# Optimization experiments

Hardware: AMD Instinct MI355X
Metric: run time of the kernel (lower is better)

## Reference

```python
import jax, jax.numpy as jnp
import numpy as np

EPS = 1e-5  # torch nn.LayerNorm default


def layer_norm(x, g, b):
    mu = jnp.mean(x, axis=-1, keepdims=True)
    var = jnp.mean(jnp.square(x - mu), axis=-1, keepdims=True)
    return (x - mu) * jax.lax.rsqrt(var + EPS) * g + b


def run_dir(g_ih_seq, w_hh, g_hh, b_hh, g_ho, b_ho, reverse):
    """Run one LayerNormLSTMCell direction over precomputed LN(x @ W_ih^T).
    g_ih_seq: [S, B, 4H]. Returns final hidden [B, H]."""
    S, B, G = g_ih_seq.shape
    H = G // 4

    def step(carry, gih_t):
        h, c = carry
        gates = gih_t + layer_norm(h @ w_hh.T, g_hh, b_hh)  # [B, 4H]
        i, f, o = jnp.split(jax.nn.sigmoid(gates[:, : 3 * H]), 3, axis=1)
        g = jnp.tanh(gates[:, 3 * H :])
        c = f * c + i * g
        h = o * jnp.tanh(layer_norm(c, g_ho, b_ho))
        return (h, c), None

    z = jnp.zeros((B, H), g_ih_seq.dtype)
    (hT, _), _ = jax.lax.scan(step, (z, z), g_ih_seq, reverse=reverse)
    return hT


def lnlstm(x, w_ih0, w_hh0, ln_ih0_g, ln_ih0_b, ln_hh0_g, ln_hh0_b, ln_ho0_g,
           ln_ho0_b, w_ih1, w_hh1, ln_ih1_g, ln_ih1_b, ln_hh1_g, ln_hh1_b,
           ln_ho1_g, ln_ho1_b):
    # x: [B, S, E] -> permute(1,0,2)
    x_seq = jnp.transpose(x, (1, 0, 2))  # [S, B, E]
    S, B, _ = x_seq.shape

    # ---- layer 0 (time-varying input) ----
    g0f = layer_norm(jnp.einsum('sbe,ge->sbg', x_seq, w_ih0[0]), ln_ih0_g[0], ln_ih0_b[0])
    hf = run_dir(g0f, w_hh0[0], ln_hh0_g[0], ln_hh0_b[0], ln_ho0_g[0], ln_ho0_b[0], False)
    g0b = layer_norm(jnp.einsum('sbe,ge->sbg', x_seq, w_ih0[1]), ln_ih0_g[1], ln_ih0_b[1])
    hb = run_dir(g0b, w_hh0[1], ln_hh0_g[1], ln_hh0_b[1], ln_ho0_g[1], ln_ho0_b[1], True)

    # Due to the `[[None]*N]*seq_len` aliasing bug in the original torch code,
    # the next layer's input is the SAME vector at every timestep:
    xc = jnp.concatenate([hf, hb], axis=1)  # [B, 2H]

    # ---- layer 1 (constant input; LN(x@W_ih^T) computed once, broadcast over time) ----
    g1f = layer_norm(xc @ w_ih1[0].T, ln_ih1_g[0], ln_ih1_b[0])
    hf1 = run_dir(jnp.broadcast_to(g1f, (S,) + g1f.shape), w_hh1[0],
                  ln_hh1_g[0], ln_hh1_b[0], ln_ho1_g[0], ln_ho1_b[0], False)
    g1b = layer_norm(xc @ w_ih1[1].T, ln_ih1_g[1], ln_ih1_b[1])
    hb1 = run_dir(jnp.broadcast_to(g1b, (S,) + g1b.shape), w_hh1[1],
                  ln_hh1_g[1], ln_hh1_b[1], ln_ho1_g[1], ln_ho1_b[1], True)

    # y = max over time of identical vectors == the vector itself
    return jnp.concatenate([hf1, hb1], axis=1)  # [B, 2H]


def setup_inputs() -> dict:
    key = jax.random.key(0)
    ks = jax.random.split(key, 20)
    B, S, E, H = 64, 48, 512, 512
    f = jnp.float32
    n = jax.random.normal
    u = jax.random.uniform
    return {
        'x': n(ks[0], (B, S, E), f),
        'text_length': jax.random.randint(ks[1], (B,), 1, S),
        'w_ih0': n(ks[2], (2, 4 * H, E), f) * 0.05,
        'w_hh0': n(ks[3], (2, 4 * H, H), f) * 0.05,
        'ln_ih0_g': u(ks[4], (2, 4 * H), f, 0.5, 1.5),
        'ln_ih0_b': n(ks[5], (2, 4 * H), f) * 0.02,
        'ln_hh0_g': u(ks[6], (2, 4 * H), f, 0.5, 1.5),
        'ln_hh0_b': n(ks[7], (2, 4 * H), f) * 0.02,
        'ln_ho0_g': u(ks[8], (2, H), f, 0.5, 1.5),
        'ln_ho0_b': n(ks[9], (2, H), f) * 0.02,
        'w_ih1': n(ks[10], (2, 4 * H, 2 * H), f) * 0.05,
        'w_hh1': n(ks[11], (2, 4 * H, H), f) * 0.05,
        'ln_ih1_g': u(ks[12], (2, 4 * H), f, 0.5, 1.5),
        'ln_ih1_b': n(ks[13], (2, 4 * H), f) * 0.02,
        'ln_hh1_g': u(ks[14], (2, 4 * H), f, 0.5, 1.5),
        'ln_hh1_b': n(ks[15], (2, 4 * H), f) * 0.02,
        'ln_ho1_g': u(ks[16], (2, H), f, 0.5, 1.5),
        'ln_ho1_b': n(ks[17], (2, H), f) * 0.02,
    }


def reference(x, text_length, w_ih0, w_hh0, ln_ih0_g, ln_ih0_b, ln_hh0_g,
              ln_hh0_b, ln_ho0_g, ln_ho0_b, w_ih1, w_hh1, ln_ih1_g, ln_ih1_b,
              ln_hh1_g, ln_hh1_b, ln_ho1_g, ln_ho1_b):
    # text_length is accepted but unused by the original forward
    return lnlstm(x, w_ih0, w_hh0, ln_ih0_g, ln_ih0_b, ln_hh0_g, ln_hh0_b,
                  ln_ho0_g, ln_ho0_b, w_ih1, w_hh1, ln_ih1_g, ln_ih1_b,
                  ln_hh1_g, ln_hh1_b, ln_ho1_g, ln_ho1_b)
```

## Files before the change

### kernel.cpp

```cpp
#include <hip/hip_runtime.h>
#include <math.h>

#define HH 512
#define BB 64
#define SS 48
#define EE 512
#define G4 2048
#define EPSF 1e-5f
#define AGENT __HIP_MEMORY_SCOPE_AGENT

__device__ __forceinline__ float aload(const float* p) {
  return __hip_atomic_load(p, __ATOMIC_RELAXED, AGENT);
}
__device__ __forceinline__ void astore(float* p, float v) {
  __hip_atomic_store(p, v, __ATOMIC_RELAXED, AGENT);
}

__device__ __forceinline__ float fsigmoid(float x) {
  float t = __builtin_amdgcn_exp2f(x * -1.44269504088896f);
  return __builtin_amdgcn_rcpf(1.f + t);
}
__device__ __forceinline__ float ftanh(float x) {
  x = fminf(fmaxf(x, -10.f), 10.f);
  float t = __builtin_amdgcn_exp2f(x * 2.88539008177793f);
  return (t - 1.f) * __builtin_amdgcn_rcpf(t + 1.f);
}

__device__ __forceinline__ void gsync(int* c, int target) {
  __builtin_amdgcn_s_waitcnt(0);
  __syncthreads();
  if (threadIdx.x == 0) {
    __hip_atomic_fetch_add(c, 1, __ATOMIC_RELEASE, AGENT);
    int spins = 0;
    while (__hip_atomic_load(c, __ATOMIC_RELAXED, AGENT) < target) {
      __builtin_amdgcn_s_sleep(2);
      if (++spins > (1 << 21)) break;
    }
    (void)__hip_atomic_load(c, __ATOMIC_ACQUIRE, AGENT);
  }
  __syncthreads();
}

__global__ __launch_bounds__(256)
void gemm_ih0(const float* __restrict__ x, const float* __restrict__ w_ih0,
              float* __restrict__ G0) {
  __shared__ float As[16][65];
  __shared__ float Bs[16][65];
  const int m0 = blockIdx.y * 64;
  const int d  = m0 / (BB * SS);
  const float* Wm = w_ih0 + (size_t)d * G4 * EE;
  const int bn = blockIdx.x * 64;
  const int tid = threadIdx.x;
  const int lrow = tid >> 2;
  const int lkk  = (tid & 3) << 2;
  const int tx = tid & 15;
  const int ty = tid >> 4;
  int m  = m0 + lrow;
  int r  = m - d * (BB * SS);
  int b  = r / SS;
  int tl = r - b * SS;
  int s  = d ? (SS - 1 - tl) : tl;
  const float* arow = x + ((size_t)b * SS + s) * EE;

  float acc[4][4] = {};
  for (int k0 = 0; k0 < EE; k0 += 16) {
    float4 av = *(const float4*)(arow + k0 + lkk);
    float4 bv = *(const float4*)(Wm + (size_t)(bn + lrow) * EE + k0 + lkk);
    As[lkk+0][lrow] = av.x; As[lkk+1][lrow] = av.y; As[lkk+2][lrow] = av.z; As[lkk+3][lrow] = av.w;
    Bs[lkk+0][lrow] = bv.x; Bs[lkk+1][lrow] = bv.y; Bs[lkk+2][lrow] = bv.z; Bs[lkk+3][lrow] = bv.w;
    __syncthreads();
    #pragma unroll
    for (int k = 0; k < 16; ++k) {
      float a[4], bbv[4];
      #pragma unroll
      for (int i = 0; i < 4; ++i) a[i] = As[k][ty*4+i];
      #pragma unroll
      for (int j = 0; j < 4; ++j) bbv[j] = Bs[k][tx*4+j];
      #pragma unroll
      for (int i = 0; i < 4; ++i)
        #pragma unroll
        for (int j = 0; j < 4; ++j) acc[i][j] += a[i]*bbv[j];
    }
    __syncthreads();
  }
  for (int i = 0; i < 4; ++i)
    for (int j = 0; j < 4; ++j)
      G0[(size_t)(m0 + ty*4 + i) * G4 + bn + tx*4 + j] = acc[i][j];
}

__global__ __launch_bounds__(256)
void ln_rows(float* __restrict__ X, const float* __restrict__ gamma,
             const float* __restrict__ beta, int rows_per_d) {
  __shared__ float red[8];
  const int row = blockIdx.x;
  const int d = row / rows_per_d;
  float* xr = X + (size_t)row * G4;
  const float* gg = gamma + (size_t)d * G4;
  const float* bb = beta  + (size_t)d * G4;
  float s = 0.f, q = 0.f;
  float v[8];
  #pragma unroll
  for (int it = 0; it < 8; ++it) {
    float xv = xr[threadIdx.x + it*256];
    v[it] = xv; s += xv; q += xv*xv;
  }
  #pragma unroll
  for (int off = 32; off > 0; off >>= 1) { s += __shfl_down(s, off); q += __shfl_down(q, off); }
  int lane = threadIdx.x & 63, wid = threadIdx.x >> 6;
  if (lane == 0) { red[wid] = s; red[4+wid] = q; }
  __syncthreads();
  float ts = red[0]+red[1]+red[2]+red[3];
  float tq = red[4]+red[5]+red[6]+red[7];
  float mu = ts * (1.f/G4);
  float rstd = rsqrtf(tq*(1.f/G4) - mu*mu + EPSF);
  #pragma unroll
  for (int it = 0; it < 8; ++it) {
    int jc = threadIdx.x + it*256;
    xr[jc] = (v[it]-mu)*rstd*gg[jc] + bb[jc];
  }
}

__global__ __launch_bounds__(1024, 4)
void persist7(const float* __restrict__ whh, const float* __restrict__ Gbuf,
              long g_row_stride, long g_t_stride,
              const float* __restrict__ lnhg, const float* __restrict__ lnhb,
              const float* __restrict__ lnog, const float* __restrict__ lnob,
              float* cbuf, float* obuf, float* Rpart, float* Cpart,
              int* flagsA, int* flagsB,
              float* fout, int nsteps,
              int mode1, const float* __restrict__ w_ih1,
              const float* __restrict__ xcb, float* g1pre,
              const float* __restrict__ ln_g1, const float* __restrict__ ln_b1,
              int* cnt_pre) {
  __shared__ float hlds[16][1024];
  __shared__ float part[16][8][64];
  __shared__ float redR[16][64];
  __shared__ float bcR[16][2];
  __shared__ float bcC[16][2];
  __shared__ float sred[32];

  const int bb = blockIdx.x;
  const int tid = threadIdx.x;

  if (mode1) {
    const int dp = bb & 1, nbp = bb >> 1;
    const int pb = tid >> 4, ns = tid & 15;
    const int col = nbp*16 + ns;
    const float* xrow = xcb + (size_t)pb * 1024;
    const float* wv_ = w_ih1 + ((size_t)dp*G4 + col) * 1024;
    float a = 0.f;
    for (int k = 0; k < 1024; k += 4) {
      float4 xv = *(const float4*)(xrow + k);
      float4 wv4 = *(const float4*)(wv_ + k);
      a += xv.x*wv4.x + xv.y*wv4.y + xv.z*wv4.z + xv.w*wv4.w;
    }
    astore(g1pre + ((size_t)dp*BB + pb) * G4 + col, a);
    gsync(cnt_pre + 0, 256);
    if (bb < 128) {
      const int ld = bb >> 6;
      float* xr = g1pre + (size_t)bb * G4;
      const float* gg = ln_g1 + (size_t)ld * G4;
      const float* be = ln_b1 + (size_t)ld * G4;
      float v0 = aload(xr + tid), v1 = aload(xr + tid + 1024);
      float s = v0 + v1, q = v0*v0 + v1*v1;
      #pragma unroll
      for (int off = 32; off > 0; off >>= 1) { s += __shfl_down(s, off); q += __shfl_down(q, off); }
      const int wv2 = tid >> 6;
      if ((tid & 63) == 0) { sred[wv2] = s; sred[16+wv2] = q; }
      __syncthreads();
      float ts = 0.f, tq = 0.f;
      #pragma unroll
      for (int i = 0; i < 16; ++i) { ts += sred[i]; tq += sred[16+i]; }
      float mu = ts * (1.f/G4);
      float rstd = rsqrtf(tq*(1.f/G4) - mu*mu + EPSF);
      astore(xr + tid,        (v0-mu)*rstd*gg[tid]      + be[tid]);
      astore(xr + tid + 1024, (v1-mu)*rstd*gg[tid+1024] + be[tid+1024]);
    }
    gsync(cnt_pre + 16, 256);
  }

  const int g  = bb & 7;
  const int d  = g >> 2;
  const int bq = g & 3;
  const int jb = bb >> 3;
  const int rowbase = d*BB + bq*16;
  const int ke = tid >> 6, nl = tid & 63;
  const int ncol = jb*16 + ((nl>>4) << 9) + (nl & 15);
  int* fA = flagsA + g*1024;
  int* fB = flagsB + g*1024;

  float wreg[32];
  {
    const float* wp = whh + ((size_t)d*G4 + ncol)*HH + (size_t)ke*32;
    #pragma unroll
    for (int i = 0; i < 32; ++i) wreg[i] = wp[i];
  }

  const int bl = tid >> 4, jl = tid & 15;
  const int rowc = rowbase + bl;
  const int jc = jb*16 + jl;
  const int scol = tid & 511, srh = tid >> 9;
  const float ogv = lnog[(size_t)d*HH + scol];
  const float obv = lnob[(size_t)d*HH + scol];
  const int row16 = tid >> 5, j32 = tid & 31;
  const int inv_g = (g_t_stride == 0);

  float hg0=0,hg1=0,hg2=0,hg3=0, hb0=0,hb1=0,hb2=0,hb3=0;
  float cg0=0,cg1=0,cg2=0,cg3=0;
  if (tid < 256) {
    const float* lnhg_d = lnhg + (size_t)d*G4;
    const float* lnhb_d = lnhb + (size_t)d*G4;
    hg0 = lnhg_d[jc];        hb0 = lnhb_d[jc];
    hg1 = lnhg_d[HH+jc];     hb1 = lnhb_d[HH+jc];
    hg2 = lnhg_d[2*HH+jc];   hb2 = lnhb_d[2*HH+jc];
    hg3 = lnhg_d[3*HH+jc];   hb3 = lnhb_d[3*HH+jc];
    if (inv_g) {
      const float* gr = Gbuf + (size_t)rowc * g_row_stride;
      cg0 = gr[jc]; cg1 = gr[HH+jc]; cg2 = gr[2*HH+jc]; cg3 = gr[3*HH+jc];
    }
  }
  float creg = 0.f;

  for (int t = 0; t < nsteps; ++t) {
    float cv[8], ovv[8];
    #pragma unroll
    for (int i = 0; i < 8; ++i) {
      int row = i*2 + srh;
      cv[i]  = aload(cbuf + (size_t)(rowbase + row)*512 + scol);
      ovv[i] = aload(obuf + (size_t)(rowbase + row)*512 + scol);
    }
    if (tid < 512) {
      float s = aload(Cpart + ((size_t)(rowbase+row16)*32 + j32)*2 + 0);
      float q = aload(Cpart + ((size_t)(rowbase+row16)*32 + j32)*2 + 1);
      #pragma unroll
      for (int off = 16; off > 0; off >>= 1) { s += __shfl_down(s, off, 32); q += __shfl_down(q, off, 32); }
      if (j32 == 0) {
        float mu = s * (1.f/HH);
        bcC[row16][0] = mu;
        bcC[row16][1] = rsqrtf(q*(1.f/HH) - mu*mu + EPSF);
      }
    }
    __syncthreads();
    #pragma unroll
    for (int i = 0; i < 8; ++i) {
      int row = i*2 + srh;
      hlds[row][scol] = ovv[i] * ftanh((cv[i] - bcC[row][0]) * bcC[row][1] * ogv + obv);
    }
    __syncthreads();

    #pragma unroll
    for (int half = 0; half < 2; ++half) {
      #pragma unroll
      for (int b = 0; b < 8; ++b) {
        const float* hp = &hlds[half*8 + b][ke*32];
        float acc = 0.f;
        #pragma unroll
        for (int i4 = 0; i4 < 8; ++i4) {
          float4 h4 = *(const float4*)(hp + 4*i4);
          acc += h4.x*wreg[4*i4+0] + h4.y*wreg[4*i4+1]
               + h4.z*wreg[4*i4+2] + h4.w*wreg[4*i4+3];
        }
        part[ke][b][nl] = acc;
      }
      __syncthreads();
      if (tid < 512) {
        int b = tid >> 6, n2 = tid & 63;
        float r = 0.f;
        #pragma unroll
        for (int k16 = 0; k16 < 16; ++k16) r += part[k16][b][n2];
        redR[half*8 + b][n2] = r;
      }
      __syncthreads();
    }
    if (tid < 512) {
      float v1 = redR[row16][j32], v2 = redR[row16][j32+32];
      float s = v1 + v2, q = v1*v1 + v2*v2;
      #pragma unroll
      for (int off = 16; off > 0; off >>= 1) { s += __shfl_down(s, off, 32); q += __shfl_down(q, off, 32); }
      if (j32 == 0) {
        astore(Rpart + ((size_t)(rowbase+row16)*32 + jb)*2 + 0, s);
        astore(Rpart + ((size_t)(rowbase+row16)*32 + jb)*2 + 1, q);
      }
    }
    float pg0 = cg0, pg1 = cg1, pg2 = cg2, pg3 = cg3;
    if (tid < 256 && !inv_g) {
      const float* gr = Gbuf + (size_t)rowc * g_row_stride + (size_t)t * g_t_stride;
      pg0 = gr[jc]; pg1 = gr[HH+jc]; pg2 = gr[2*HH+jc]; pg3 = gr[3*HH+jc];
    }
    __syncthreads();
    if (tid == 0) __hip_atomic_store(fA + jb*32, t + 1, __ATOMIC_RELAXED, AGENT);
    if (tid < 32) {
      int spins = 0;
      for (;;) {
        int v = __hip_atomic_load(fA + tid*32, __ATOMIC_RELAXED, AGENT);
        #pragma unroll
        for (int off = 16; off > 0; off >>= 1) v = min(v, __shfl_down(v, off, 32));
        v = __shfl(v, 0, 32);
        if (v >= t + 1) break;
        __builtin_amdgcn_s_sleep(1);
        if (++spins > (1 << 22)) break;
      }
    }
    __syncthreads();

    if (tid < 512) {
      float s = aload(Rpart + ((size_t)(rowbase+row16)*32 + j32)*2 + 0);
      float q = aload(Rpart + ((size_t)(rowbase+row16)*32 + j32)*2 + 1);
      #pragma unroll
      for (int off = 16; off > 0; off >>= 1) { s += __shfl_down(s, off, 32); q += __shfl_down(q, off, 32); }
      if (j32 == 0) {
        float mu = s * (1.f/G4);
        bcR[row16][0] = mu;
        bcR[row16][1] = rsqrtf(q*(1.f/G4) - mu*mu + EPSF);
      }
    }
    __syncthreads();

    if (tid < 256) {
      float mu = bcR[bl][0], rstd = bcR[bl][1];
      float gi = pg0 + (redR[bl][jl]    - mu)*rstd*hg0 + hb0;
      float gf = pg1 + (redR[bl][16+jl] - mu)*rstd*hg1 + hb1;
      float go = pg2 + (redR[bl][32+jl] - mu)*rstd*hg2 + hb2;
      float gt = pg3 + (redR[bl][48+jl] - mu)*rstd*hg3 + hb3;
      float iv = fsigmoid(gi), fv = fsigmoid(gf);
      float ov = fsigmoid(go), gv = ftanh(gt);
      creg = fv*creg + iv*gv;
      float cs = creg, cq = creg*creg;
      #pragma unroll
      for (int off = 8; off > 0; off >>= 1) { cs += __shfl_down(cs, off, 16); cq += __shfl_down(cq, off, 16); }
      if (jl == 0) {
        astore(Cpart + ((size_t)rowc*32 + jb)*2 + 0, cs);
        astore(Cpart + ((size_t)rowc*32 + jb)*2 + 1, cq);
      }
      astore(cbuf + (size_t)rowc*512 + jc, creg);
      astore(obuf + (size_t)rowc*512 + jc, ov);
    }
    __syncthreads();
    if (tid == 0) __hip_atomic_store(fB + jb*32, t + 1, __ATOMIC_RELAXED, AGENT);
    if (tid < 32) {
      int spins = 0;
      for (;;) {
        int v = __hip_atomic_load(fB + tid*32, __ATOMIC_RELAXED, AGENT);
        #pragma unroll
        for (int off = 16; off > 0; off >>= 1) v = min(v, __shfl_down(v, off, 32));
        v = __shfl(v, 0, 32);
        if (v >= t + 1) break;
        __builtin_amdgcn_s_sleep(1);
        if (++spins > (1 << 22)) break;
      }
    }
    __syncthreads();
  }

  {
    float cv[8], ovv[8];
    #pragma unroll
    for (int i = 0; i < 8; ++i) {
      int row = i*2 + srh;
      cv[i]  = aload(cbuf + (size_t)(rowbase + row)*512 + scol);
      ovv[i] = aload(obuf + (size_t)(rowbase + row)*512 + scol);
    }
    if (tid < 512) {
      float s = aload(Cpart + ((size_t)(rowbase+row16)*32 + j32)*2 + 0);
      float q = aload(Cpart + ((size_t)(rowbase+row16)*32 + j32)*2 + 1);
      #pragma unroll
      for (int off = 16; off > 0; off >>= 1) { s += __shfl_down(s, off, 32); q += __shfl_down(q, off, 32); }
      if (j32 == 0) {
        float mu = s * (1.f/HH);
        bcC[row16][0] = mu;
        bcC[row16][1] = rsqrtf(q*(1.f/HH) - mu*mu + EPSF);
      }
    }
    __syncthreads();
    if (jb == 0) {
      #pragma unroll
      for (int i = 0; i < 8; ++i) {
        int row = i*2 + srh;
        float h = ovv[i] * ftanh((cv[i] - bcC[row][0]) * bcC[row][1] * ogv + obv);
        fout[(size_t)(bq*16 + row) * 1024 + (size_t)d*512 + scol] = h;
      }
    }
  }
}

extern "C" void kernel_launch(void* const* d_in, const int* in_sizes, int n_in,
                              void* d_out, int out_size, void* d_ws, size_t ws_size,
                              hipStream_t stream) {
  const float* x        = (const float*)d_in[0];
  const float* w_ih0    = (const float*)d_in[2];
  const float* w_hh0    = (const float*)d_in[3];
  const float* ln_ih0_g = (const float*)d_in[4];
  const float* ln_ih0_b = (const float*)d_in[5];
  const float* ln_hh0_g = (const float*)d_in[6];
  const float* ln_hh0_b = (const float*)d_in[7];
  const float* ln_ho0_g = (const float*)d_in[8];
  const float* ln_ho0_b = (const float*)d_in[9];
  const float* w_ih1    = (const float*)d_in[10];
  const float* w_hh1    = (const float*)d_in[11];
  const float* ln_ih1_g = (const float*)d_in[12];
  const float* ln_ih1_b = (const float*)d_in[13];
  const float* ln_hh1_g = (const float*)d_in[14];
  const float* ln_hh1_b = (const float*)d_in[15];
  const float* ln_ho1_g = (const float*)d_in[16];
  const float* ln_ho1_b = (const float*)d_in[17];
  float* out = (float*)d_out;

  float* G0    = (float*)d_ws;
  float* g1pre = G0 + (size_t)2*BB*SS*G4;
  float* xcb   = g1pre + (size_t)2*BB*G4;
  float* Rpart = xcb + (size_t)BB*1024;
  float* Cpart = Rpart + (size_t)128*32*2;
  float* cbuf  = Cpart + (size_t)128*32*2;
  float* obuf  = cbuf + (size_t)128*512;
  int*   ints  = (int*)(obuf + (size_t)128*512);
  int*   fA0     = ints;
  int*   fB0     = ints + 8192;
  int*   fA1     = ints + 16384;
  int*   fB1     = ints + 24576;
  int*   cnt_pre = ints + 32768;

  hipMemsetAsync(Cpart, 0, ((size_t)128*32*2 + 2*(size_t)128*512)*sizeof(float)
                           + 32832*sizeof(int), stream);

  hipLaunchKernelGGL(gemm_ih0, dim3(G4/64, (2*BB*SS)/64), dim3(256), 0, stream,
      x, w_ih0, G0);
  hipLaunchKernelGGL(ln_rows, dim3(2*BB*SS), dim3(256), 0, stream,
      G0, ln_ih0_g, ln_ih0_b, BB*SS);

  hipLaunchKernelGGL(persist7, dim3(256), dim3(1024), 0, stream,
      w_hh0, G0, (long)SS*G4, (long)G4,
      ln_hh0_g, ln_hh0_b, ln_ho0_g, ln_ho0_b,
      cbuf, obuf, Rpart, Cpart, fA0, fB0, xcb, SS,
      0, (const float*)nullptr, (const float*)nullptr, (float*)nullptr,
      (const float*)nullptr, (const float*)nullptr, (int*)nullptr);

  hipMemsetAsync(Cpart, 0, ((size_t)128*32*2 + 2*(size_t)128*512)*sizeof(float), stream);

  hipLaunchKernelGGL(persist7, dim3(256), dim3(1024), 0, stream,
      w_hh1, g1pre, (long)G4, 0L,
      ln_hh1_g, ln_hh1_b, ln_ho1_g, ln_ho1_b,
      cbuf, obuf, Rpart, Cpart, fA1, fB1, out, SS,
      1, w_ih1, xcb, g1pre, ln_ih1_g, ln_ih1_b, cnt_pre);
}
```

Baseline: 1.752 ms.

## Replace flag barriers with timestep-tagged data packets for fine-grained sync

The separate flag arrays and block-wide barrier spins after each phase are removed. Each published value (partial LN sums and the c/o state) is now written as a 16-byte packet that carries a timestep tag, stored with cache-bypassing inline asm. Consumers poll the data itself until the tag reaches the current step, so each thread waits only on the values it needs. This aims to cut two grid-wide barrier round trips per step, at the cost of larger 4x-padded buffers, spin-polling many vector loads, and relying on the 16-byte stores being observed atomically.

```diff
diff --git a/kernel.cpp b/kernel.cpp
--- a/kernel.cpp
+++ b/kernel.cpp
@@ -9,11 +9,46 @@
 #define EPSF 1e-5f
 #define AGENT __HIP_MEMORY_SCOPE_AGENT
 
+typedef __attribute__((ext_vector_type(4))) float f32x4;
+
 __device__ __forceinline__ float aload(const float* p) {
   return __hip_atomic_load(p, __ATOMIC_RELAXED, AGENT);
 }
 __device__ __forceinline__ void astore(float* p, float v) {
   __hip_atomic_store(p, v, __ATOMIC_RELAXED, AGENT);
+}
+
+__device__ __forceinline__ f32x4 ld4c(const float* p) {
+  f32x4 v;
+  asm volatile("global_load_dwordx4 %0, %1, off sc0 sc1\n\ts_waitcnt vmcnt(0)"
+               : "=&v"(v) : "v"(p) : "memory");
+  return v;
+}
+__device__ __forceinline__ void st4c(float* p, float a, float b, float tg) {
+  f32x4 v; v.x = a; v.y = b; v.z = tg; v.w = 0.f;
+  asm volatile("global_store_dwordx4 %0, %1, off sc0 sc1"
+               :: "v"(p), "v"(v) : "memory");
+}
+__device__ __forceinline__ void ld8c(
+    const float* p0, const float* p1, const float* p2, const float* p3,
+    const float* p4, const float* p5, const float* p6, const float* p7,
+    f32x4& r0, f32x4& r1, f32x4& r2, f32x4& r3,
+    f32x4& r4, f32x4& r5, f32x4& r6, f32x4& r7) {
+  asm volatile(
+      "global_load_dwordx4 %0, %8, off sc0 sc1\n\t"
+      "global_load_dwordx4 %1, %9, off sc0 sc1\n\t"
+      "global_load_dwordx4 %2, %10, off sc0 sc1\n\t"
+      "global_load_dwordx4 %3, %11, off sc0 sc1\n\t"
+      "global_load_dwordx4 %4, %12, off sc0 sc1\n\t"
+      "global_load_dwordx4 %5, %13, off sc0 sc1\n\t"
+      "global_load_dwordx4 %6, %14, off sc0 sc1\n\t"
+      "global_load_dwordx4 %7, %15, off sc0 sc1\n\t"
+      "s_waitcnt vmcnt(0)"
+      : "=&v"(r0), "=&v"(r1), "=&v"(r2), "=&v"(r3),
+        "=&v"(r4), "=&v"(r5), "=&v"(r6), "=&v"(r7)
+      : "v"(p0), "v"(p1), "v"(p2), "v"(p3),
+        "v"(p4), "v"(p5), "v"(p6), "v"(p7)
+      : "memory");
 }
 
 __device__ __forceinline__ float fsigmoid(float x) {
@@ -121,12 +156,11 @@
 }
 
 __global__ __launch_bounds__(1024, 4)
-void persist7(const float* __restrict__ whh, const float* __restrict__ Gbuf,
+void persist8(const float* __restrict__ whh, const float* __restrict__ Gbuf,
               long g_row_stride, long g_t_stride,
               const float* __restrict__ lnhg, const float* __restrict__ lnhb,
               const float* __restrict__ lnog, const float* __restrict__ lnob,
-              float* cbuf, float* obuf, float* Rpart, float* Cpart,
-              int* flagsA, int* flagsB,
+              float* cot, float* Rp4, float* Cp4,
               float* fout, int nsteps,
               int mode1, const float* __restrict__ w_ih1,
               const float* __restrict__ xcb, float* g1pre,
@@ -186,8 +220,6 @@
   const int rowbase = d*BB + bq*16;
   const int ke = tid >> 6, nl = tid & 63;
   const int ncol = jb*16 + ((nl>>4) << 9) + (nl & 15);
-  int* fA = flagsA + g*1024;
-  int* fB = flagsB + g*1024;
 
   float wreg[32];
   {
@@ -204,6 +236,13 @@
   const float obv = lnob[(size_t)d*HH + scol];
   const int row16 = tid >> 5, j32 = tid & 31;
   const int inv_g = (g_t_stride == 0);
+
+  const float* pcs  = cot + ((size_t)((rowbase + srh)*512 + scol) << 2);
+  const float* cpp4 = Cp4 + ((size_t)((rowbase + row16)*32 + j32) << 2);
+  const float* rpp4 = Rp4 + ((size_t)((rowbase + row16)*32 + j32) << 2);
+  float* rpub4 = Rp4 + ((size_t)((rowbase + row16)*32 + jb) << 2);
+  float* cpub4 = Cp4 + ((size_t)(rowc*32 + jb) << 2);
+  float* cwp4  = cot + ((size_t)(rowc*512 + jc) << 2);
 
   float hg0=0,hg1=0,hg2=0,hg3=0, hb0=0,hb1=0,hb2=0,hb3=0;
   float cg0=0,cg1=0,cg2=0,cg3=0;
@@ -221,17 +260,32 @@
   }
   float creg = 0.f;
 
-  for (int t = 0; t < nsteps; ++t) {
-    float cv[8], ovv[8];
-    #pragma unroll
-    for (int i = 0; i < 8; ++i) {
-      int row = i*2 + srh;
-      cv[i]  = aload(cbuf + (size_t)(rowbase + row)*512 + scol);
-      ovv[i] = aload(obuf + (size_t)(rowbase + row)*512 + scol);
+  for (int t = 0; t <= nsteps; ++t) {
+    const float ft = (float)t;
+    f32x4 r0,r1,r2,r3,r4,r5,r6,r7;
+    ld8c(pcs, pcs+4096, pcs+2*4096, pcs+3*4096,
+         pcs+4*4096, pcs+5*4096, pcs+6*4096, pcs+7*4096,
+         r0,r1,r2,r3,r4,r5,r6,r7);
+    {
+      int spins = 0;
+      while (fminf(fminf(fminf(r0.z,r1.z),fminf(r2.z,r3.z)),
+                   fminf(fminf(r4.z,r5.z),fminf(r6.z,r7.z))) < ft) {
+        __builtin_amdgcn_s_sleep(1);
+        ld8c(pcs, pcs+4096, pcs+2*4096, pcs+3*4096,
+             pcs+4*4096, pcs+5*4096, pcs+6*4096, pcs+7*4096,
+             r0,r1,r2,r3,r4,r5,r6,r7);
+        if (++spins > (1 << 20)) break;
+      }
     }
     if (tid < 512) {
-      float s = aload(Cpart + ((size_t)(rowbase+row16)*32 + j32)*2 + 0);
-      float q = aload(Cpart + ((size_t)(rowbase+row16)*32 + j32)*2 + 1);
+      f32x4 cp = ld4c(cpp4);
+      int spins = 0;
+      while (cp.z < ft) {
+        __builtin_amdgcn_s_sleep(1);
+        cp = ld4c(cpp4);
+        if (++spins > (1 << 20)) break;
+      }
+      float s = cp.x, q = cp.y;
       #pragma unroll
       for (int off = 16; off > 0; off >>= 1) { s += __shfl_down(s, off, 32); q += __shfl_down(q, off, 32); }
       if (j32 == 0) {
@@ -241,10 +295,28 @@
       }
     }
     __syncthreads();
-    #pragma unroll
-    for (int i = 0; i < 8; ++i) {
-      int row = i*2 + srh;
-      hlds[row][scol] = ovv[i] * ftanh((cv[i] - bcC[row][0]) * bcC[row][1] * ogv + obv);
+    {
+      float cv[8], ovv[8];
+      cv[0]=r0.x; cv[1]=r1.x; cv[2]=r2.x; cv[3]=r3.x;
+      cv[4]=r4.x; cv[5]=r5.x; cv[6]=r6.x; cv[7]=r7.x;
+      ovv[0]=r0.y; ovv[1]=r1.y; ovv[2]=r2.y; ovv[3]=r3.y;
+      ovv[4]=r4.y; ovv[5]=r5.y; ovv[6]=r6.y; ovv[7]=r7.y;
+      if (t == nsteps) {
+        if (jb == 0) {
+          #pragma unroll
+          for (int i = 0; i < 8; ++i) {
+            int row = i*2 + srh;
+            float h = ovv[i] * ftanh((cv[i] - bcC[row][0]) * bcC[row][1] * ogv + obv);
+            fout[(size_t)(bq*16 + row) * 1024 + (size_t)d*512 + scol] = h;
+          }
+        }
+        break;
+      }
+      #pragma unroll
+      for (int i = 0; i < 8; ++i) {
+        int row = i*2 + srh;
+        hlds[row][scol] = ovv[i] * ftanh((cv[i] - bcC[row][0]) * bcC[row][1] * ogv + obv);
+      }
     }
     __syncthreads();
 
@@ -277,35 +349,22 @@
       float s = v1 + v2, q = v1*v1 + v2*v2;
       #pragma unroll
       for (int off = 16; off > 0; off >>= 1) { s += __shfl_down(s, off, 32); q += __shfl_down(q, off, 32); }
-      if (j32 == 0) {
-        astore(Rpart + ((size_t)(rowbase+row16)*32 + jb)*2 + 0, s);
-        astore(Rpart + ((size_t)(rowbase+row16)*32 + jb)*2 + 1, q);
-      }
+      if (j32 == 0) st4c(rpub4, s, q, ft + 1.f);
     }
     float pg0 = cg0, pg1 = cg1, pg2 = cg2, pg3 = cg3;
     if (tid < 256 && !inv_g) {
       const float* gr = Gbuf + (size_t)rowc * g_row_stride + (size_t)t * g_t_stride;
       pg0 = gr[jc]; pg1 = gr[HH+jc]; pg2 = gr[2*HH+jc]; pg3 = gr[3*HH+jc];
     }
-    __syncthreads();
-    if (tid == 0) __hip_atomic_store(fA + jb*32, t + 1, __ATOMIC_RELAXED, AGENT);
-    if (tid < 32) {
+    if (tid < 512) {
+      f32x4 rp = ld4c(rpp4);
       int spins = 0;
-      for (;;) {
-        int v = __hip_atomic_load(fA + tid*32, __ATOMIC_RELAXED, AGENT);
-        #pragma unroll
-        for (int off = 16; off > 0; off >>= 1) v = min(v, __shfl_down(v, off, 32));
-        v = __shfl(v, 0, 32);
-        if (v >= t + 1) break;
+      while (rp.z < ft + 1.f) {
         __builtin_amdgcn_s_sleep(1);
-        if (++spins > (1 << 22)) break;
-      }
-    }
-    __syncthreads();
-
-    if (tid < 512) {
-      float s = aload(Rpart + ((size_t)(rowbase+row16)*32 + j32)*2 + 0);
-      float q = aload(Rpart + ((size_t)(rowbase+row16)*32 + j32)*2 + 1);
+        rp = ld4c(rpp4);
+        if (++spins > (1 << 20)) break;
+      }
+      float s = rp.x, q = rp.y;
       #pragma unroll
       for (int off = 16; off > 0; off >>= 1) { s += __shfl_down(s, off, 32); q += __shfl_down(q, off, 32); }
       if (j32 == 0) {
@@ -328,57 +387,8 @@
       float cs = creg, cq = creg*creg;
       #pragma unroll
       for (int off = 8; off > 0; off >>= 1) { cs += __shfl_down(cs, off, 16); cq += __shfl_down(cq, off, 16); }
-      if (jl == 0) {
-        astore(Cpart + ((size_t)rowc*32 + jb)*2 + 0, cs);
-        astore(Cpart + ((size_t)rowc*32 + jb)*2 + 1, cq);
-      }
-      astore(cbuf + (size_t)rowc*512 + jc, creg);
-      astore(obuf + (size_t)rowc*512 + jc, ov);
-    }
-    __syncthreads();
-    if (tid == 0) __hip_atomic_store(fB + jb*32, t + 1, __ATOMIC_RELAXED, AGENT);
-    if (tid < 32) {
-      int spins = 0;
-      for (;;) {
-        int v = __hip_atomic_load(fB + tid*32, __ATOMIC_RELAXED, AGENT);
-        #pragma unroll
-        for (int off = 16; off > 0; off >>= 1) v = min(v, __shfl_down(v, off, 32));
-        v = __shfl(v, 0, 32);
-        if (v >= t + 1) break;
-        __builtin_amdgcn_s_sleep(1);
-        if (++spins > (1 << 22)) break;
-      }
-    }
-    __syncthreads();
-  }
-
-  {
-    float cv[8], ovv[8];
-    #pragma unroll
-    for (int i = 0; i < 8; ++i) {
-      int row = i*2 + srh;
-      cv[i]  = aload(cbuf + (size_t)(rowbase + row)*512 + scol);
-      ovv[i] = aload(obuf + (size_t)(rowbase + row)*512 + scol);
-    }
-    if (tid < 512) {
-      float s = aload(Cpart + ((size_t)(rowbase+row16)*32 + j32)*2 + 0);
-      float q = aload(Cpart + ((size_t)(rowbase+row16)*32 + j32)*2 + 1);
-      #pragma unroll
-      for (int off = 16; off > 0; off >>= 1) { s += __shfl_down(s, off, 32); q += __shfl_down(q, off, 32); }
-      if (j32 == 0) {
-        float mu = s * (1.f/HH);
-        bcC[row16][0] = mu;
-        bcC[row16][1] = rsqrtf(q*(1.f/HH) - mu*mu + EPSF);
-      }
-    }
-    __syncthreads();
-    if (jb == 0) {
-      #pragma unroll
-      for (int i = 0; i < 8; ++i) {
-        int row = i*2 + srh;
-        float h = ovv[i] * ftanh((cv[i] - bcC[row][0]) * bcC[row][1] * ogv + obv);
-        fout[(size_t)(bq*16 + row) * 1024 + (size_t)d*512 + scol] = h;
-      }
+      if (jl == 0) st4c(cpub4, cs, cq, ft + 1.f);
+      st4c(cwp4, creg, ov, ft + 1.f);
     }
   }
 }
@@ -408,37 +418,32 @@
   float* G0    = (float*)d_ws;
   float* g1pre = G0 + (size_t)2*BB*SS*G4;
   float* xcb   = g1pre + (size_t)2*BB*G4;
-  float* Rpart = xcb + (size_t)BB*1024;
-  float* Cpart = Rpart + (size_t)128*32*2;
-  float* cbuf  = Cpart + (size_t)128*32*2;
-  float* obuf  = cbuf + (size_t)128*512;
-  int*   ints  = (int*)(obuf + (size_t)128*512);
-  int*   fA0     = ints;
-  int*   fB0     = ints + 8192;
-  int*   fA1     = ints + 16384;
-  int*   fB1     = ints + 24576;
-  int*   cnt_pre = ints + 32768;
-
-  hipMemsetAsync(Cpart, 0, ((size_t)128*32*2 + 2*(size_t)128*512)*sizeof(float)
-                           + 32832*sizeof(int), stream);
+  float* Rp4   = xcb + (size_t)BB*1024;
+  float* Cp4   = Rp4 + (size_t)128*32*4;
+  float* cot   = Cp4 + (size_t)128*32*4;
+  int*   cnt_pre = (int*)(cot + (size_t)128*512*4);
+
+  const size_t zr_floats = (size_t)128*32*4 *2 + (size_t)128*512*4;
+
+  hipMemsetAsync(Rp4, 0, zr_floats*sizeof(float) + 64*sizeof(int), stream);
 
   hipLaunchKernelGGL(gemm_ih0, dim3(G4/64, (2*BB*SS)/64), dim3(256), 0, stream,
       x, w_ih0, G0);
   hipLaunchKernelGGL(ln_rows, dim3(2*BB*SS), dim3(256), 0, stream,
       G0, ln_ih0_g, ln_ih0_b, BB*SS);
 
-  hipLaunchKernelGGL(persist7, dim3(256), dim3(1024), 0, stream,
+  hipLaunchKernelGGL(persist8, dim3(256), dim3(1024), 0, stream,
       w_hh0, G0, (long)SS*G4, (long)G4,
       ln_hh0_g, ln_hh0_b, ln_ho0_g, ln_ho0_b,
-      cbuf, obuf, Rpart, Cpart, fA0, fB0, xcb, SS,
+      cot, Rp4, Cp4, xcb, SS,
       0, (const float*)nullptr, (const float*)nullptr, (float*)nullptr,
       (const float*)nullptr, (const float*)nullptr, (int*)nullptr);
 
-  hipMemsetAsync(Cpart, 0, ((size_t)128*32*2 + 2*(size_t)128*512)*sizeof(float), stream);
-
-  hipLaunchKernelGGL(persist7, dim3(256), dim3(1024), 0, stream,
+  hipMemsetAsync(Rp4, 0, zr_floats*sizeof(float), stream);
+
+  hipLaunchKernelGGL(persist8, dim3(256), dim3(1024), 0, stream,
       w_hh1, g1pre, (long)G4, 0L,
       ln_hh1_g, ln_hh1_b, ln_ho1_g, ln_ho1_b,
-      cbuf, obuf, Rpart, Cpart, fA1, fB1, out, SS,
+      cot, Rp4, Cp4, out, SS,
       1, w_ih1, xcb, g1pre, ln_ih1_g, ln_ih1_b, cnt_pre);
 }
```

Result: slower. 1.958 ms (+11.8%).

## Split persistent LSTM kernel across 512 blocks of 512 threads

Applied to the files above, without the earlier changes.

Reworks the persistent recurrent kernel from 256 blocks of 1024 threads to 512 blocks of 512 threads. Each block now owns 8 hidden columns instead of 16, and the flag barrier spans 64 blocks per group instead of 32. The aim is to spread the recurrent matvec over more CUs and cut per-block reduction passes, for example by dropping the two-half loop. In exchange each step reads twice as many partial LayerNorm statistics, and every barrier has to wait on more flag participants.

```diff
diff --git a/kernel.cpp b/kernel.cpp
--- a/kernel.cpp
+++ b/kernel.cpp
@@ -37,6 +37,24 @@
       if (++spins > (1 << 21)) break;
     }
     (void)__hip_atomic_load(c, __ATOMIC_ACQUIRE, AGENT);
+  }
+  __syncthreads();
+}
+
+__device__ __forceinline__ void flagbar(int* f, int jb, int t1, int tid) {
+  __syncthreads();
+  if (tid == 0) __hip_atomic_store(f + jb*32, t1, __ATOMIC_RELAXED, AGENT);
+  if (tid < 64) {
+    int spins = 0;
+    for (;;) {
+      int v = __hip_atomic_load(f + tid*32, __ATOMIC_RELAXED, AGENT);
+      #pragma unroll
+      for (int off = 32; off > 0; off >>= 1) v = min(v, __shfl_down(v, off));
+      v = __shfl(v, 0);
+      if (v >= t1) break;
+      __builtin_amdgcn_s_sleep(1);
+      if (++spins > (1 << 22)) break;
+    }
   }
   __syncthreads();
 }
@@ -120,8 +138,8 @@
   }
 }
 
-__global__ __launch_bounds__(1024, 4)
-void persist7(const float* __restrict__ whh, const float* __restrict__ Gbuf,
+__global__ __launch_bounds__(512, 4)
+void persist9(const float* __restrict__ whh, const float* __restrict__ Gbuf,
               long g_row_stride, long g_t_stride,
               const float* __restrict__ lnhg, const float* __restrict__ lnhb,
               const float* __restrict__ lnog, const float* __restrict__ lnob,
@@ -132,20 +150,20 @@
               const float* __restrict__ xcb, float* g1pre,
               const float* __restrict__ ln_g1, const float* __restrict__ ln_b1,
               int* cnt_pre) {
-  __shared__ float hlds[16][1024];
-  __shared__ float part[16][8][64];
-  __shared__ float redR[16][64];
+  __shared__ float hlds[16][512];
+  __shared__ float part[16][16][33];
+  __shared__ float redR[16][33];
   __shared__ float bcR[16][2];
   __shared__ float bcC[16][2];
-  __shared__ float sred[32];
+  __shared__ float sred[16];
 
   const int bb = blockIdx.x;
   const int tid = threadIdx.x;
 
   if (mode1) {
     const int dp = bb & 1, nbp = bb >> 1;
-    const int pb = tid >> 4, ns = tid & 15;
-    const int col = nbp*16 + ns;
+    const int pb = tid >> 3, ns = tid & 7;
+    const int col = nbp*8 + ns;
     const float* xrow = xcb + (size_t)pb * 1024;
     const float* wv_ = w_ih1 + ((size_t)dp*G4 + col) * 1024;
     float a = 0.f;
@@ -155,39 +173,44 @@
       a += xv.x*wv4.x + xv.y*wv4.y + xv.z*wv4.z + xv.w*wv4.w;
     }
     astore(g1pre + ((size_t)dp*BB + pb) * G4 + col, a);
-    gsync(cnt_pre + 0, 256);
+    gsync(cnt_pre + 0, 512);
     if (bb < 128) {
       const int ld = bb >> 6;
       float* xr = g1pre + (size_t)bb * G4;
       const float* gg = ln_g1 + (size_t)ld * G4;
       const float* be = ln_b1 + (size_t)ld * G4;
-      float v0 = aload(xr + tid), v1 = aload(xr + tid + 1024);
-      float s = v0 + v1, q = v0*v0 + v1*v1;
+      float v0 = aload(xr + tid),        v1 = aload(xr + tid + 512);
+      float v2 = aload(xr + tid + 1024), v3 = aload(xr + tid + 1536);
+      float s = v0+v1+v2+v3, q = v0*v0+v1*v1+v2*v2+v3*v3;
       #pragma unroll
       for (int off = 32; off > 0; off >>= 1) { s += __shfl_down(s, off); q += __shfl_down(q, off); }
       const int wv2 = tid >> 6;
-      if ((tid & 63) == 0) { sred[wv2] = s; sred[16+wv2] = q; }
+      if ((tid & 63) == 0) { sred[wv2] = s; sred[8+wv2] = q; }
       __syncthreads();
       float ts = 0.f, tq = 0.f;
       #pragma unroll
-      for (int i = 0; i < 16; ++i) { ts += sred[i]; tq += sred[16+i]; }
+      for (int i = 0; i < 8; ++i) { ts += sred[i]; tq += sred[8+i]; }
       float mu = ts * (1.f/G4);
       float rstd = rsqrtf(tq*(1.f/G4) - mu*mu + EPSF);
       astore(xr + tid,        (v0-mu)*rstd*gg[tid]      + be[tid]);
-      astore(xr + tid + 1024, (v1-mu)*rstd*gg[tid+1024] + be[tid+1024]);
-    }
-    gsync(cnt_pre + 16, 256);
-  }
-
-  const int g  = bb & 7;
+      astore(xr + tid + 512,  (v1-mu)*rstd*gg[tid+512]  + be[tid+512]);
+      astore(xr + tid + 1024, (v2-mu)*rstd*gg[tid+1024] + be[tid+1024]);
+      astore(xr + tid + 1536, (v3-mu)*rstd*gg[tid+1536] + be[tid+1536]);
+    }
+    gsync(cnt_pre + 16, 512);
+  }
+
+  const int g  = (bb & 3) | (((bb >> 8) & 1) << 2);
+  const int jb = (bb >> 2) & 63;
   const int d  = g >> 2;
   const int bq = g & 3;
-  const int jb = bb >> 3;
   const int rowbase = d*BB + bq*16;
-  const int ke = tid >> 6, nl = tid & 63;
-  const int ncol = jb*16 + ((nl>>4) << 9) + (nl & 15);
-  int* fA = flagsA + g*1024;
-  int* fB = flagsB + g*1024;
+  int* fA = flagsA + g*2048;
+  int* fB = flagsB + g*2048;
+
+  const int ke  = tid >> 5;
+  const int n32 = tid & 31;
+  const int ncol = jb*8 + ((n32 >> 3) << 9) + (n32 & 7);
 
   float wreg[32];
   {
@@ -196,18 +219,17 @@
     for (int i = 0; i < 32; ++i) wreg[i] = wp[i];
   }
 
-  const int bl = tid >> 4, jl = tid & 15;
-  const int rowc = rowbase + bl;
-  const int jc = jb*16 + jl;
-  const int scol = tid & 511, srh = tid >> 9;
-  const float ogv = lnog[(size_t)d*HH + scol];
-  const float obv = lnob[(size_t)d*HH + scol];
+  const int bl = tid >> 3, jl = tid & 7;
+  const int rowc = rowbase + (bl & 15);
+  const int jc = jb*8 + jl;
+  const float ogv = lnog[(size_t)d*HH + tid];
+  const float obv = lnob[(size_t)d*HH + tid];
   const int row16 = tid >> 5, j32 = tid & 31;
   const int inv_g = (g_t_stride == 0);
 
   float hg0=0,hg1=0,hg2=0,hg3=0, hb0=0,hb1=0,hb2=0,hb3=0;
   float cg0=0,cg1=0,cg2=0,cg3=0;
-  if (tid < 256) {
+  if (tid < 128) {
     const float* lnhg_d = lnhg + (size_t)d*G4;
     const float* lnhb_d = lnhb + (size_t)d*G4;
     hg0 = lnhg_d[jc];        hb0 = lnhb_d[jc];
@@ -222,16 +244,17 @@
   float creg = 0.f;
 
   for (int t = 0; t < nsteps; ++t) {
-    float cv[8], ovv[8];
-    #pragma unroll
-    for (int i = 0; i < 8; ++i) {
-      int row = i*2 + srh;
-      cv[i]  = aload(cbuf + (size_t)(rowbase + row)*512 + scol);
-      ovv[i] = aload(obuf + (size_t)(rowbase + row)*512 + scol);
-    }
-    if (tid < 512) {
-      float s = aload(Cpart + ((size_t)(rowbase+row16)*32 + j32)*2 + 0);
-      float q = aload(Cpart + ((size_t)(rowbase+row16)*32 + j32)*2 + 1);
+    float cv[16], ovv[16];
+    #pragma unroll
+    for (int i = 0; i < 16; ++i) {
+      cv[i]  = aload(cbuf + (size_t)(rowbase + i)*512 + tid);
+      ovv[i] = aload(obuf + (size_t)(rowbase + i)*512 + tid);
+    }
+    {
+      float s = aload(Cpart + ((size_t)(rowbase+row16)*64 + j32)*2 + 0)
+              + aload(Cpart + ((size_t)(rowbase+row16)*64 + j32 + 32)*2 + 0);
+      float q = aload(Cpart + ((size_t)(rowbase+row16)*64 + j32)*2 + 1)
+              + aload(Cpart + ((size_t)(rowbase+row16)*64 + j32 + 32)*2 + 1);
       #pragma unroll
       for (int off = 16; off > 0; off >>= 1) { s += __shfl_down(s, off, 32); q += __shfl_down(q, off, 32); }
       if (j32 == 0) {
@@ -242,70 +265,48 @@
     }
     __syncthreads();
     #pragma unroll
-    for (int i = 0; i < 8; ++i) {
-      int row = i*2 + srh;
-      hlds[row][scol] = ovv[i] * ftanh((cv[i] - bcC[row][0]) * bcC[row][1] * ogv + obv);
-    }
-    __syncthreads();
-
-    #pragma unroll
-    for (int half = 0; half < 2; ++half) {
-      #pragma unroll
-      for (int b = 0; b < 8; ++b) {
-        const float* hp = &hlds[half*8 + b][ke*32];
-        float acc = 0.f;
-        #pragma unroll
-        for (int i4 = 0; i4 < 8; ++i4) {
-          float4 h4 = *(const float4*)(hp + 4*i4);
-          acc += h4.x*wreg[4*i4+0] + h4.y*wreg[4*i4+1]
-               + h4.z*wreg[4*i4+2] + h4.w*wreg[4*i4+3];
-        }
-        part[ke][b][nl] = acc;
-      }
-      __syncthreads();
-      if (tid < 512) {
-        int b = tid >> 6, n2 = tid & 63;
-        float r = 0.f;
-        #pragma unroll
-        for (int k16 = 0; k16 < 16; ++k16) r += part[k16][b][n2];
-        redR[half*8 + b][n2] = r;
-      }
-      __syncthreads();
-    }
-    if (tid < 512) {
-      float v1 = redR[row16][j32], v2 = redR[row16][j32+32];
-      float s = v1 + v2, q = v1*v1 + v2*v2;
+    for (int i = 0; i < 16; ++i)
+      hlds[i][tid] = ovv[i] * ftanh((cv[i] - bcC[i][0]) * bcC[i][1] * ogv + obv);
+    __syncthreads();
+
+    #pragma unroll
+    for (int b = 0; b < 16; ++b) {
+      const float* hp = &hlds[b][ke*32];
+      float acc = 0.f;
+      #pragma unroll
+      for (int i4 = 0; i4 < 8; ++i4) {
+        float4 h4 = *(const float4*)(hp + 4*i4);
+        acc += h4.x*wreg[4*i4+0] + h4.y*wreg[4*i4+1]
+             + h4.z*wreg[4*i4+2] + h4.w*wreg[4*i4+3];
+      }
+      part[ke][b][n32] = acc;
+    }
+    __syncthreads();
+    {
+      float r = 0.f;
+      #pragma unroll
+      for (int k16 = 0; k16 < 16; ++k16) r += part[k16][row16][n32];
+      redR[row16][n32] = r;
+      float s = r, q = r*r;
       #pragma unroll
       for (int off = 16; off > 0; off >>= 1) { s += __shfl_down(s, off, 32); q += __shfl_down(q, off, 32); }
-      if (j32 == 0) {
-        astore(Rpart + ((size_t)(rowbase+row16)*32 + jb)*2 + 0, s);
-        astore(Rpart + ((size_t)(rowbase+row16)*32 + jb)*2 + 1, q);
+      if (n32 == 0) {
+        astore(Rpart + ((size_t)(rowbase+row16)*64 + jb)*2 + 0, s);
+        astore(Rpart + ((size_t)(rowbase+row16)*64 + jb)*2 + 1, q);
       }
     }
     float pg0 = cg0, pg1 = cg1, pg2 = cg2, pg3 = cg3;
-    if (tid < 256 && !inv_g) {
+    if (tid < 128 && !inv_g) {
       const float* gr = Gbuf + (size_t)rowc * g_row_stride + (size_t)t * g_t_stride;
       pg0 = gr[jc]; pg1 = gr[HH+jc]; pg2 = gr[2*HH+jc]; pg3 = gr[3*HH+jc];
     }
-    __syncthreads();
-    if (tid == 0) __hip_atomic_store(fA + jb*32, t + 1, __ATOMIC_RELAXED, AGENT);
-    if (tid < 32) {
-      int spins = 0;
-      for (;;) {
-        int v = __hip_atomic_load(fA + tid*32, __ATOMIC_RELAXED, AGENT);
-        #pragma unroll
-        for (int off = 16; off > 0; off >>= 1) v = min(v, __shfl_down(v, off, 32));
-        v = __shfl(v, 0, 32);
-        if (v >= t + 1) break;
-        __builtin_amdgcn_s_sleep(1);
-        if (++spins > (1 << 22)) break;
-      }
-    }
-    __syncthreads();
-
-    if (tid < 512) {
-      float s = aload(Rpart + ((size_t)(rowbase+row16)*32 + j32)*2 + 0);
-      float q = aload(Rpart + ((size_t)(rowbase+row16)*32 + j32)*2 + 1);
+    flagbar(fA, jb, t + 1, tid);
+
+    {
+      float s = aload(Rpart + ((size_t)(rowbase+row16)*64 + j32)*2 + 0)
+              + aload(Rpart + ((size_t)(rowbase+row16)*64 + j32 + 32)*2 + 0);
+      float q = aload(Rpart + ((size_t)(rowbase+row16)*64 + j32)*2 + 1)
+              + aload(Rpart + ((size_t)(rowbase+row16)*64 + j32 + 32)*2 + 1);
       #pragma unroll
       for (int off = 16; off > 0; off >>= 1) { s += __shfl_down(s, off, 32); q += __shfl_down(q, off, 32); }
       if (j32 == 0) {
@@ -316,53 +317,40 @@
     }
     __syncthreads();
 
-    if (tid < 256) {
+    if (tid < 128) {
       float mu = bcR[bl][0], rstd = bcR[bl][1];
-      float gi = pg0 + (redR[bl][jl]    - mu)*rstd*hg0 + hb0;
-      float gf = pg1 + (redR[bl][16+jl] - mu)*rstd*hg1 + hb1;
-      float go = pg2 + (redR[bl][32+jl] - mu)*rstd*hg2 + hb2;
-      float gt = pg3 + (redR[bl][48+jl] - mu)*rstd*hg3 + hb3;
+      float gi = pg0 + (redR[bl][jl]      - mu)*rstd*hg0 + hb0;
+      float gf = pg1 + (redR[bl][8+jl]    - mu)*rstd*hg1 + hb1;
+      float go = pg2 + (redR[bl][16+jl]   - mu)*rstd*hg2 + hb2;
+      float gt = pg3 + (redR[bl][24+jl]   - mu)*rstd*hg3 + hb3;
       float iv = fsigmoid(gi), fv = fsigmoid(gf);
       float ov = fsigmoid(go), gv = ftanh(gt);
       creg = fv*creg + iv*gv;
       float cs = creg, cq = creg*creg;
       #pragma unroll
-      for (int off = 8; off > 0; off >>= 1) { cs += __shfl_down(cs, off, 16); cq += __shfl_down(cq, off, 16); }
+      for (int off = 4; off > 0; off >>= 1) { cs += __shfl_down(cs, off, 8); cq += __shfl_down(cq, off, 8); }
       if (jl == 0) {
-        astore(Cpart + ((size_t)rowc*32 + jb)*2 + 0, cs);
-        astore(Cpart + ((size_t)rowc*32 + jb)*2 + 1, cq);
+        astore(Cpart + ((size_t)rowc*64 + jb)*2 + 0, cs);
+        astore(Cpart + ((size_t)rowc*64 + jb)*2 + 1, cq);
       }
       astore(cbuf + (size_t)rowc*512 + jc, creg);
       astore(obuf + (size_t)rowc*512 + jc, ov);
     }
-    __syncthreads();
-    if (tid == 0) __hip_atomic_store(fB + jb*32, t + 1, __ATOMIC_RELAXED, AGENT);
-    if (tid < 32) {
-      int spins = 0;
-      for (;;) {
-        int v = __hip_atomic_load(fB + tid*32, __ATOMIC_RELAXED, AGENT);
-        #pragma unroll
-        for (int off = 16; off > 0; off >>= 1) v = min(v, __shfl_down(v, off, 32));
-        v = __shfl(v, 0, 32);
-        if (v >= t + 1) break;
-        __builtin_amdgcn_s_sleep(1);
-        if (++spins > (1 << 22)) break;
-      }
-    }
-    __syncthreads();
+    flagbar(fB, jb, t + 1, tid);
   }
 
   {
-    float cv[8], ovv[8];
-    #pragma unroll
-    for (int i = 0; i < 8; ++i) {
-      int row = i*2 + srh;
-      cv[i]  = aload(cbuf + (size_t)(rowbase + row)*512 + scol);
-      ovv[i] = aload(obuf + (size_t)(rowbase + row)*512 + scol);
-    }
-    if (tid < 512) {
-      float s = aload(Cpart + ((size_t)(rowbase+row16)*32 + j32)*2 + 0);
-      float q = aload(Cpart + ((size_t)(rowbase+row16)*32 + j32)*2 + 1);
+    float cv[16], ovv[16];
+    #pragma unroll
+    for (int i = 0; i < 16; ++i) {
+      cv[i]  = aload(cbuf + (size_t)(rowbase + i)*512 + tid);
+      ovv[i] = aload(obuf + (size_t)(rowbase + i)*512 + tid);
+    }
+    {
+      float s = aload(Cpart + ((size_t)(rowbase+row16)*64 + j32)*2 + 0)
+              + aload(Cpart + ((size_t)(rowbase+row16)*64 + j32 + 32)*2 + 0);
+      float q = aload(Cpart + ((size_t)(rowbase+row16)*64 + j32)*2 + 1)
+              + aload(Cpart + ((size_t)(rowbase+row16)*64 + j32 + 32)*2 + 1);
       #pragma unroll
       for (int off = 16; off > 0; off >>= 1) { s += __shfl_down(s, off, 32); q += __shfl_down(q, off, 32); }
       if (j32 == 0) {
@@ -374,10 +362,9 @@
     __syncthreads();
     if (jb == 0) {
       #pragma unroll
-      for (int i = 0; i < 8; ++i) {
-        int row = i*2 + srh;
-        float h = ovv[i] * ftanh((cv[i] - bcC[row][0]) * bcC[row][1] * ogv + obv);
-        fout[(size_t)(bq*16 + row) * 1024 + (size_t)d*512 + scol] = h;
+      for (int i = 0; i < 16; ++i) {
+        float h = ovv[i] * ftanh((cv[i] - bcC[i][0]) * bcC[i][1] * ogv + obv);
+        fout[(size_t)(bq*16 + i) * 1024 + (size_t)d*512 + tid] = h;
       }
     }
   }
@@ -409,34 +396,34 @@
   float* g1pre = G0 + (size_t)2*BB*SS*G4;
   float* xcb   = g1pre + (size_t)2*BB*G4;
   float* Rpart = xcb + (size_t)BB*1024;
-  float* Cpart = Rpart + (size_t)128*32*2;
-  float* cbuf  = Cpart + (size_t)128*32*2;
+  float* Cpart = Rpart + (size_t)128*64*2;
+  float* cbuf  = Cpart + (size_t)128*64*2;
   float* obuf  = cbuf + (size_t)128*512;
   int*   ints  = (int*)(obuf + (size_t)128*512);
   int*   fA0     = ints;
-  int*   fB0     = ints + 8192;
-  int*   fA1     = ints + 16384;
-  int*   fB1     = ints + 24576;
-  int*   cnt_pre = ints + 32768;
-
-  hipMemsetAsync(Cpart, 0, ((size_t)128*32*2 + 2*(size_t)128*512)*sizeof(float)
-                           + 32832*sizeof(int), stream);
+  int*   fB0     = ints + 16384;
+  int*   fA1     = ints + 32768;
+  int*   fB1     = ints + 49152;
+  int*   cnt_pre = ints + 65536;
+
+  hipMemsetAsync(Cpart, 0, ((size_t)128*64*2 + 2*(size_t)128*512)*sizeof(float)
+                           + 65600*sizeof(int), stream);
 
   hipLaunchKernelGGL(gemm_ih0, dim3(G4/64, (2*BB*SS)/64), dim3(256), 0, stream,
       x, w_ih0, G0);
   hipLaunchKernelGGL(ln_rows, dim3(2*BB*SS), dim3(256), 0, stream,
       G0, ln_ih0_g, ln_ih0_b, BB*SS);
 
-  hipLaunchKernelGGL(persist7, dim3(256), dim3(1024), 0, stream,
+  hipLaunchKernelGGL(persist9, dim3(512), dim3(512), 0, stream,
       w_hh0, G0, (long)SS*G4, (long)G4,
       ln_hh0_g, ln_hh0_b, ln_ho0_g, ln_ho0_b,
       cbuf, obuf, Rpart, Cpart, fA0, fB0, xcb, SS,
       0, (const float*)nullptr, (const float*)nullptr, (float*)nullptr,
       (const float*)nullptr, (const float*)nullptr, (int*)nullptr);
 
-  hipMemsetAsync(Cpart, 0, ((size_t)128*32*2 + 2*(size_t)128*512)*sizeof(float), stream);
-
-  hipLaunchKernelGGL(persist7, dim3(256), dim3(1024), 0, stream,
+  hipMemsetAsync(Cpart, 0, ((size_t)128*64*2 + 2*(size_t)128*512)*sizeof(float), stream);
+
+  hipLaunchKernelGGL(persist9, dim3(512), dim3(512), 0, stream,
       w_hh1, g1pre, (long)G4, 0L,
       ln_hh1_g, ln_hh1_b, ln_ho1_g, ln_ho1_b,
       cbuf, obuf, Rpart, Cpart, fA1, fB1, out, SS,
```

New measurement: 2.766 ms. +57.9%, slower.
